# Performance work log

Hardware: AMD Instinct MI355X
Metric: run time of the kernel (lower is better)

Reference implementation:

```python
import jax, jax.numpy as jnp
import numpy as np

DIM = 512
CODEBOOK_SIZE = 8192
B, N = 4, 4096


def setup_inputs() -> dict:
    key = jax.random.key(0)
    k1, k2, k3 = jax.random.split(key, 3)
    scale = DIM ** -0.5
    x = jax.random.normal(k1, (B, N, DIM), dtype=jnp.float32)
    codebook = jax.random.normal(k2, (CODEBOOK_SIZE, DIM), dtype=jnp.float32) * scale
    W = jax.random.normal(k3, (DIM, DIM), dtype=jnp.float32) * scale  # Linear(dim, dim, bias=False) weight
    return {"x": x, "codebook": codebook, "W": W}


def reference(x, codebook, W):
    # implicit_codebook = Linear(codebook): codebook @ W.T   -> [C, D]
    implicit = codebook @ W.T

    # nearest-code search (no grad in original): squared euclidean distance
    x_sg = jax.lax.stop_gradient(x)
    imp_sg = jax.lax.stop_gradient(implicit)
    # [B, N, C] logits; ||x||^2 constant w.r.t. argmin so omitted
    d2 = jnp.sum(imp_sg * imp_sg, axis=-1) - 2.0 * jnp.einsum("bnd,cd->bnc", x_sg, imp_sg)
    indices = jnp.argmin(d2, axis=-1)  # [B, N]

    quantized = implicit[indices]  # gather [B, N, D]

    commit_loss = (
        0.25 * jnp.mean((x - jax.lax.stop_gradient(quantized)) ** 2)
        + jnp.mean((jax.lax.stop_gradient(x) - quantized) ** 2)
    )

    # straight-through estimator
    quantized_st = jax.lax.stop_gradient(quantized - x) + x
    return quantized_st, indices, commit_loss
```

## Files before the change

### kernel.cpp

```cpp
#include <hip/hip_runtime.h>
#include <stdint.h>

#define DIM 512
#define NCODE 8192
#define NTOK 16384
#define QELEMS (NTOK * DIM)
#define IDX_OFF QELEMS
#define LOSS_OFF (QELEMS + NTOK)

#define S_X 21.166666f
#define S_I 423.33334f
#define SXSI 8960.5551f
#define NQ_BIAS 131072
#define MARGIN_INT 3136

#define OFF_NORMS ((size_t)NCODE * DIM * 4)
#define OFF_XI8   (OFF_NORMS + (size_t)NCODE * 4)
#define OFF_II8   (OFF_XI8 + (size_t)NTOK * DIM)
#define OFF_CAND  (OFF_II8 + (size_t)NCODE * DIM)
#define OFF_NQ    (OFF_CAND + (size_t)NTOK * 64 * 4 * 4)

typedef short bf16x8 __attribute__((ext_vector_type(8)));
typedef float f32x4 __attribute__((ext_vector_type(4)));
typedef int   i32x4 __attribute__((ext_vector_type(4)));

__device__ inline unsigned ord32(float f) {
    unsigned u = __float_as_uint(f);
    return (u & 0x80000000u) ? ~u : (u | 0x80000000u);
}
__device__ inline unsigned short f2bf(float f) {
    unsigned u = __float_as_uint(f);
    return (unsigned short)((u + 0x7fffu + ((u >> 16) & 1u)) >> 16);
}
__device__ inline float bf2f(unsigned short h) {
    return __uint_as_float((unsigned)h << 16);
}
__device__ inline int q8(float v, float s) {
    return __float2int_rn(fminf(fmaxf(v * s, -127.f), 127.f));
}
__device__ inline void gl_lds16(const void* g, void* l) {
    __builtin_amdgcn_global_load_lds(
        (const __attribute__((address_space(1))) void*)g,
        (__attribute__((address_space(3))) void*)l, 16, 0, 0);
}

__device__ inline void leaf4(const uint4 v, unsigned r[4]) {
    const unsigned s0 = min(v.x, v.z), t0 = max(v.x, v.z);
    const unsigned s1 = min(v.y, v.w), t1 = max(v.y, v.w);
    r[0] = s0; r[1] = min(t0, s1); r[2] = max(t0, s1); r[3] = t1;
}
__device__ inline void merge44(unsigned a[4], const unsigned b[4]) {
    const unsigned h0 = min(a[0], b[3]), h1 = min(a[1], b[2]);
    const unsigned h2 = min(a[2], b[1]), h3 = min(a[3], b[0]);
    const unsigned l0 = min(h0, h2), u0 = max(h0, h2);
    const unsigned l1 = min(h1, h3), u1 = max(h1, h3);
    a[0] = min(l0, l1); a[1] = max(l0, l1);
    a[2] = min(u0, u1); a[3] = max(u0, u1);
}

__global__ void init_kernel(float* __restrict__ norms) {
    int i = blockIdx.x * blockDim.x + threadIdx.x;
    if (i < NCODE) norms[i] = 0.f;
}

__global__ void split_kernel(const float* __restrict__ src,
                             unsigned short* __restrict__ dst, int n4) {
    int i = blockIdx.x * blockDim.x + threadIdx.x;
    if (i >= n4) return;
    float4 v = ((const float4*)src)[i];
    int r = i >> 7;
    int c = (i & 127) << 2;
    unsigned short hx = f2bf(v.x), hy = f2bf(v.y), hz = f2bf(v.z), hw = f2bf(v.w);
    ushort4 hi = {hx, hy, hz, hw};
    ushort4 lo = {f2bf(v.x - bf2f(hx)), f2bf(v.y - bf2f(hy)),
                  f2bf(v.z - bf2f(hz)), f2bf(v.w - bf2f(hw))};
    *(ushort4*)(dst + (size_t)r * 1024 + c) = hi;
    *(ushort4*)(dst + (size_t)r * 1024 + 512 + c) = lo;
}

__global__ __launch_bounds__(256, 2)
void gemm_imp_kernel(const unsigned short* __restrict__ A2,
                     const unsigned short* __restrict__ B2,
                     float* __restrict__ imp, unsigned char* __restrict__ impi8,
                     float* __restrict__ norms) {
    __shared__ __align__(16) unsigned short As2[64 * 64];
    __shared__ __align__(16) unsigned short Bs2[128 * 64];
    const int tid = threadIdx.x;
    const int l = tid & 63;
    const int w = tid >> 6;
    const int row0 = blockIdx.y * 64;
    const int col0 = blockIdx.x * 128;
    const int lr = l & 15;
    const int q = l >> 4;

    const int rr8 = l >> 3;
    const int gch = (l & 7) ^ (rr8 & 7);

    const unsigned short* gA = A2 + (size_t)(row0 + w * 8 + rr8) * 1024 + gch * 8;
    const unsigned short* gB = B2 + (size_t)(col0 + w * 8 + rr8) * 1024 + gch * 8;
    unsigned short* lA = As2 + (w * 8) * 64;
    unsigned short* lB = Bs2 + (w * 8) * 64;

    f32x4 acc[4][2];
    #pragma unroll
    for (int i = 0; i < 4; ++i)
        #pragma unroll
        for (int j = 0; j < 2; ++j) acc[i][j] = (f32x4)0.f;

    for (int c = 0; c < 32; ++c) {
        const int kA = (c & 15) << 6;
        const int kB = (c < 16) ? kA : ((kA + 512) & 1023);
        #pragma unroll
        for (int s = 0; s < 2; ++s)
            gl_lds16(gA + (size_t)(s * 32) * 1024 + kA, lA + (s * 32) * 64);
        #pragma unroll
        for (int s = 0; s < 4; ++s)
            gl_lds16(gB + (size_t)(s * 32) * 1024 + kB, lB + (s * 32) * 64);
        __syncthreads();
        #pragma unroll
        for (int ks = 0; ks < 2; ++ks) {
            const int lc = ks * 4 + q;
            bf16x8 af[4], bf[2];
            #pragma unroll
            for (int i = 0; i < 4; ++i) {
                const int ra = i * 16 + lr;
                af[i] = *(const bf16x8*)(As2 + ra * 64 + ((lc ^ (ra & 7)) << 3));
            }
            #pragma unroll
            for (int j = 0; j < 2; ++j) {
                const int rb = w * 32 + j * 16 + lr;
                bf[j] = *(const bf16x8*)(Bs2 + rb * 64 + ((lc ^ (rb & 7)) << 3));
            }
            #pragma unroll
            for (int i = 0; i < 4; ++i)
                #pragma unroll
                for (int j = 0; j < 2; ++j)
                    acc[i][j] = __builtin_amdgcn_mfma_f32_16x16x32_bf16(
                        af[i], bf[j], acc[i][j], 0, 0, 0);
        }
        __syncthreads();
    }

    #pragma unroll
    for (int i = 0; i < 4; ++i) {
        float np[4] = {0.f, 0.f, 0.f, 0.f};
        #pragma unroll
        for (int j = 0; j < 2; ++j) {
            const int col = col0 + w * 32 + j * 16 + lr;
            #pragma unroll
            for (int r = 0; r < 4; ++r) {
                const int row = row0 + i * 16 + q * 4 + r;
                const float v = acc[i][j][r];
                imp[(size_t)row * DIM + col] = v;
                impi8[(size_t)row * DIM + col] = (unsigned char)(q8(v, S_I) & 0xff);
                np[r] = fmaf(v, v, np[r]);
            }
        }
        #pragma unroll
        for (int r = 0; r < 4; ++r) {
            float s = np[r];
            #pragma unroll
            for (int m = 1; m < 16; m <<= 1) s += __shfl_xor(s, m, 64);
            if (lr == 0)
                atomicAdd(&norms[row0 + i * 16 + q * 4 + r], s);
        }
    }
}

__global__ void cvtx_kernel(const float* __restrict__ src,
                            unsigned char* __restrict__ dst,
                            const float* __restrict__ norms,
                            int* __restrict__ norms_q, int n4) {
    int i = blockIdx.x * blockDim.x + threadIdx.x;
    if (i >= n4) return;
    if (i < NCODE) norms_q[i] = __float2int_rn(norms[i] * SXSI) + NQ_BIAS;
    float4 v = ((const float4*)src)[i];
    unsigned wd = (unsigned)(q8(v.x, S_X) & 0xff)
                | ((unsigned)(q8(v.y, S_X) & 0xff) << 8)
                | ((unsigned)(q8(v.z, S_X) & 0xff) << 16)
                | ((unsigned)(q8(v.w, S_X) & 0xff) << 24);
    ((unsigned*)dst)[i] = wd;
}

__global__ __launch_bounds__(256, 4)
void coarse_kernel(const unsigned char* __restrict__ Xi8,
                   const unsigned char* __restrict__ Ii8,
                   const int* __restrict__ norms_q,
                   unsigned* __restrict__ cand) {
    __shared__ __align__(16) unsigned char smem[32768];
    unsigned char* As = smem;
    unsigned char* Bsm = smem + 16384;
    unsigned* Sw = (unsigned*)smem;

    const int tid = threadIdx.x;
    const int l = tid & 63;
    const int w = tid >> 6;

    const int id = blockIdx.y * 64 + blockIdx.x;
    const int xcd = id & 7;
    const int s8 = id >> 3;
    const int bx = xcd * 8 + (s8 & 7);
    const int by = s8 >> 3;
    const int row0 = by * 128;
    const int col0 = bx * 128;

    const int wm = w & 1, wn = w >> 1;
    const int lr = l & 15;
    const int q = l >> 4;

    const int rr8 = l >> 3;
    const int ch = (l & 7) ^ (rr8 & 7);
    const unsigned char* gA = Xi8 + (size_t)(row0 + w * 32 + rr8) * DIM + ch * 16;
    const unsigned char* gB = Ii8 + (size_t)(col0 + w * 32 + rr8) * DIM + ch * 16;
    unsigned char* lA = As + (w * 32) * 128;
    unsigned char* lB = Bsm + (w * 32) * 128;

    i32x4 acc[4][4];
    #pragma unroll
    for (int i = 0; i < 4; ++i)
        #pragma unroll
        for (int j = 0; j < 4; ++j) acc[i][j] = (i32x4)0;

    for (int kc = 0; kc < DIM; kc += 128) {
        #pragma unroll
        for (int s = 0; s < 4; ++s) {
            gl_lds16(gA + (size_t)(s * 8) * DIM + kc, lA + (s * 8) * 128);
            gl_lds16(gB + (size_t)(s * 8) * DIM + kc, lB + (s * 8) * 128);
        }
        __syncthreads();
        #pragma unroll
        for (int ks = 0; ks < 2; ++ks) {
            i32x4 af[4], bfr[4];
            #pragma unroll
            for (int i = 0; i < 4; ++i)
                af[i] = *(const i32x4*)(
                    As + (wm * 64 + i * 16 + lr) * 128 +
                    (((ks * 4 + q) ^ (lr & 7)) << 4));
            #pragma unroll
            for (int j = 0; j < 4; ++j)
                bfr[j] = *(const i32x4*)(
                    Bsm + (wn * 64 + j * 16 + lr) * 128 +
                    (((ks * 4 + q) ^ (lr & 7)) << 4));
            #pragma unroll
            for (int i = 0; i < 4; ++i)
                #pragma unroll
                for (int j = 0; j < 4; ++j)
                    acc[i][j] = __builtin_amdgcn_mfma_i32_16x16x64_i8(
                        af[i], bfr[j], acc[i][j], 0, 0, 0);
        }
        __syncthreads();
    }

    int nqo[4];
    unsigned codes[4];
    #pragma unroll
    for (int j = 0; j < 4; ++j) {
        codes[j] = (unsigned)(col0 + wn * 64 + j * 16 + lr);
        nqo[j] = norms_q[codes[j]];
    }
    const int c4w = wn * 8 + (lr >> 1);
    const int wsub = (lr & 1) << 1;
    #pragma unroll
    for (int i = 0; i < 4; ++i) {
        #pragma unroll
        for (int r = 0; r < 4; ++r) {
            unsigned pv[4];
            #pragma unroll
            for (int j = 0; j < 4; ++j) {
                int d2o = nqo[j] - 2 * acc[i][j][r];
                d2o = min(max(d2o, 0), 262143);
                pv[j] = ((unsigned)d2o << 13) | codes[j];
            }
            const unsigned s1 = min(pv[0], pv[1]), g1 = max(pv[0], pv[1]);
            const unsigned s2 = min(pv[2], pv[3]), g2 = max(pv[2], pv[3]);
            uint2 o;
            o.x = min(s1, s2);
            o.y = min(max(s1, s2), min(g1, g2));
            const int tok = wm * 64 + i * 16 + q * 4 + r;
            *(uint2*)(Sw + tok * 64 + ((c4w ^ (tok & 7)) << 2) + wsub) = o;
        }
    }
    __syncthreads();

    {
        const int t = tid >> 1, h = tid & 1;
        const unsigned* rowp = Sw + t * 64;
        const int sxor = t & 7;
        unsigned a4[4], b4[4];
        {
            const uint4 va = *(const uint4*)(rowp + (((h * 8 + 0) ^ sxor) << 2));
            const uint4 vb = *(const uint4*)(rowp + (((h * 8 + 1) ^ sxor) << 2));
            leaf4(va, a4); leaf4(vb, b4); merge44(a4, b4);
        }
        #pragma unroll
        for (int p = 1; p < 4; ++p) {
            unsigned c4a[4], c4b[4];
            const uint4 va = *(const uint4*)(rowp + (((h * 8 + 2 * p) ^ sxor) << 2));
            const uint4 vb = *(const uint4*)(rowp + (((h * 8 + 2 * p + 1) ^ sxor) << 2));
            leaf4(va, c4a); leaf4(vb, c4b); merge44(c4a, c4b);
            merge44(a4, c4a);
        }
        const unsigned p0 = (unsigned)__shfl_xor((int)a4[0], 1, 64);
        const unsigned p1 = (unsigned)__shfl_xor((int)a4[1], 1, 64);
        const unsigned p2 = (unsigned)__shfl_xor((int)a4[2], 1, 64);
        const unsigned p3 = (unsigned)__shfl_xor((int)a4[3], 1, 64);
        if (!h) {
            uint4 o;
            o.x = min(a4[0], p3); o.y = min(a4[1], p2);
            o.z = min(a4[2], p1); o.w = min(a4[3], p0);
            *(uint4*)(cand + ((size_t)bx * NTOK + row0 + t) * 4) = o;
        }
    }
}

__global__ __launch_bounds__(256)
void merge_kernel(const float* __restrict__ X, const float* __restrict__ Imp,
                  const float* __restrict__ norms, const unsigned* __restrict__ cand,
                  float* __restrict__ out, float* __restrict__ lossp) {
    const int t = blockIdx.x * 4 + (threadIdx.x >> 6);
    const int l = threadIdx.x & 63;

    const uint4 c4 = *(const uint4*)(cand + ((size_t)l * NTOK + t) * 4);
    unsigned mn = min(min(c4.x, c4.y), min(c4.z, c4.w));
    #pragma unroll
    for (int o = 32; o > 0; o >>= 1)
        mn = min(mn, (unsigned)__shfl_xor((int)mn, o, 64));
    const unsigned th = (mn >> 13) + MARGIN_INT;

    const float4* xp = (const float4*)(X + (size_t)t * DIM);
    const float4 xa = xp[l * 2], xb = xp[l * 2 + 1];

    const unsigned vv[4] = {c4.x, c4.y, c4.z, c4.w};
    unsigned long long best = ~0ull;
    #pragma unroll
    for (int i = 0; i < 4; ++i) {
        const bool pass = (vv[i] >> 13) <= th;
        unsigned long long m = __ballot(pass);
        while (m) {
            const int src = __ffsll((unsigned long long)m) - 1;
            m &= m - 1;
            const int c = __shfl((int)(vv[i] & 8191u), src, 64);
            const float4* ip = (const float4*)(Imp + (size_t)c * DIM);
            const float4 ia = ip[l * 2], ib = ip[l * 2 + 1];
            float s = xa.x * ia.x + xa.y * ia.y + xa.z * ia.z + xa.w * ia.w
                    + xb.x * ib.x + xb.y * ib.y + xb.z * ib.z + xb.w * ib.w;
            #pragma unroll
            for (int o = 32; o > 0; o >>= 1) s += __shfl_xor(s, o, 64);
            const float d = fmaf(-2.f, s, norms[c]);
            const unsigned long long p =
                ((unsigned long long)ord32(d) << 32) | (unsigned)c;
            if (p < best) best = p;
        }
    }
    const int bi = (int)(best & 0xffffffffu);

    const float4* qp = (const float4*)(Imp + (size_t)bi * DIM);
    float4* op = (float4*)(out + (size_t)t * DIM);
    float ls = 0.f;
    #pragma unroll
    for (int jj = 0; jj < 2; ++jj) {
        const int j = l + jj * 64;
        const float4 qv = qp[j], xv = xp[j];
        op[j] = qv;
        const float dx = xv.x - qv.x, dy = xv.y - qv.y,
                    dz = xv.z - qv.z, dw = xv.w - qv.w;
        ls += dx * dx + dy * dy + dz * dz + dw * dw;
    }
    #pragma unroll
    for (int o = 32; o > 0; o >>= 1) ls += __shfl_xor(ls, o, 64);
    if (l == 0) {
        lossp[t] = ls;
        out[IDX_OFF + t] = (float)bi;
    }
}

__global__ __launch_bounds__(1024)
void fin_kernel(const float* __restrict__ lossp, float* __restrict__ out) {
    __shared__ float part[16];
    float s = 0.f;
    for (int i = threadIdx.x; i < NTOK; i += 1024) s += lossp[i];
    #pragma unroll
    for (int o = 32; o > 0; o >>= 1) s += __shfl_xor(s, o, 64);
    if ((threadIdx.x & 63) == 0) part[threadIdx.x >> 6] = s;
    __syncthreads();
    if (threadIdx.x == 0) {
        float tot = 0.f;
        #pragma unroll
        for (int i = 0; i < 16; ++i) tot += part[i];
        out[LOSS_OFF] = 1.25f * tot / (float)QELEMS;
    }
}

extern "C" void kernel_launch(void* const* d_in, const int* in_sizes, int n_in,
                              void* d_out, int out_size, void* d_ws, size_t ws_size,
                              hipStream_t stream) {
    const float* x  = (const float*)d_in[0];
    const float* cb = (const float*)d_in[1];
    const float* W  = (const float*)d_in[2];
    float* out = (float*)d_out;
    char* ws = (char*)d_ws;

    float* imp = (float*)ws;
    float* norms = (float*)(ws + OFF_NORMS);
    unsigned char* xi8 = (unsigned char*)(ws + OFF_XI8);
    unsigned char* ii8 = (unsigned char*)(ws + OFF_II8);
    unsigned* cand = (unsigned*)(ws + OFF_CAND);
    int* norms_q = (int*)(ws + OFF_NQ);
    unsigned short* cb2 = (unsigned short*)(ws + OFF_CAND);
    unsigned short* W2  = (unsigned short*)(ws + OFF_XI8);
    float* lossp = (float*)(ws + OFF_XI8);

    hipLaunchKernelGGL(init_kernel, dim3(NCODE / 256), dim3(256), 0, stream, norms);
    hipLaunchKernelGGL(split_kernel, dim3(NCODE * 128 / 256), dim3(256), 0, stream,
                       cb, cb2, NCODE * 128);
    hipLaunchKernelGGL(split_kernel, dim3(512 * 128 / 256), dim3(256), 0, stream,
                       W, W2, 512 * 128);
    hipLaunchKernelGGL(gemm_imp_kernel, dim3(DIM / 128, NCODE / 64), dim3(256), 0,
                       stream, cb2, W2, imp, ii8, norms);
    hipLaunchKernelGGL(cvtx_kernel, dim3(NTOK * DIM / 4 / 256), dim3(256), 0, stream,
                       x, xi8, norms, norms_q, NTOK * DIM / 4);
    hipLaunchKernelGGL(coarse_kernel, dim3(NCODE / 128, NTOK / 128), dim3(256), 0,
                       stream, xi8, ii8, norms_q, cand);
    hipLaunchKernelGGL(merge_kernel, dim3(NTOK / 4), dim3(256), 0, stream,
                       x, imp, norms, cand, out, lossp);
    hipLaunchKernelGGL(fin_kernel, dim3(1), dim3(1024), 0, stream, lossp, out);
}
```

Before: 262.2 us.

## Double-buffer int8 coarse GEMM K-loop with prefetch and new LDS layout

Restructures the int8 MFMA coarse distance kernel so the K loop runs in 64-byte chunks. The two halves of the 32KB shared buffer are ping-ponged, and the next chunk's global-to-LDS loads are issued before the current chunk's MFMAs, so load latency can hide behind compute. The load and read addressing is reworked to a paired-row swizzled layout. The launch bound hint rises from 4 to 5 blocks per CU. The epilogue now uses two lane shuffles instead of four, with both lanes writing half of the top-4 candidate result. Risks are more register pressure under the tighter occupancy bound and possible LDS bank conflicts from the new layout.

```diff
diff --git a/kernel.cpp b/kernel.cpp
--- a/kernel.cpp
+++ b/kernel.cpp
@@ -182,14 +182,12 @@
     ((unsigned*)dst)[i] = wd;
 }
 
-__global__ __launch_bounds__(256, 4)
+__global__ __launch_bounds__(256, 5)
 void coarse_kernel(const unsigned char* __restrict__ Xi8,
                    const unsigned char* __restrict__ Ii8,
                    const int* __restrict__ norms_q,
                    unsigned* __restrict__ cand) {
     __shared__ __align__(16) unsigned char smem[32768];
-    unsigned char* As = smem;
-    unsigned char* Bsm = smem + 16384;
     unsigned* Sw = (unsigned*)smem;
 
     const int tid = threadIdx.x;
@@ -208,12 +206,20 @@
     const int lr = l & 15;
     const int q = l >> 4;
 
-    const int rr8 = l >> 3;
-    const int ch = (l & 7) ^ (rr8 & 7);
-    const unsigned char* gA = Xi8 + (size_t)(row0 + w * 32 + rr8) * DIM + ch * 16;
-    const unsigned char* gB = Ii8 + (size_t)(col0 + w * 32 + rr8) * DIM + ch * 16;
-    unsigned char* lA = As + (w * 32) * 128;
-    unsigned char* lB = Bsm + (w * 32) * 128;
+    const int sl = l >> 3;
+    const int eq = (l & 7) ^ sl;
+    const int se = eq >> 2;
+    const int sq = eq & 3;
+    const unsigned char* gA0 =
+        Xi8 + (size_t)(row0 + 2 * (w * 8 + sl) + se) * DIM + sq * 16;
+    const unsigned char* gB0 =
+        Ii8 + (size_t)(col0 + 2 * (w * 8 + sl) + se) * DIM + sq * 16;
+    const int ldsA = w * 1024;
+    const int ldsB = 8192 + w * 1024;
+
+    const int p8 = ((((lr & 1) << 2) | q) ^ ((lr >> 1) & 7)) << 4;
+    const int rdA = (wm * 32 + (lr >> 1)) * 128 + p8;
+    const int rdB = 8192 + (wn * 32 + (lr >> 1)) * 128 + p8;
 
     i32x4 acc[4][4];
     #pragma unroll
@@ -221,33 +227,38 @@
         #pragma unroll
         for (int j = 0; j < 4; ++j) acc[i][j] = (i32x4)0;
 
-    for (int kc = 0; kc < DIM; kc += 128) {
-        #pragma unroll
-        for (int s = 0; s < 4; ++s) {
-            gl_lds16(gA + (size_t)(s * 8) * DIM + kc, lA + (s * 8) * 128);
-            gl_lds16(gB + (size_t)(s * 8) * DIM + kc, lB + (s * 8) * 128);
-        }
-        __syncthreads();
-        #pragma unroll
-        for (int ks = 0; ks < 2; ++ks) {
-            i32x4 af[4], bfr[4];
-            #pragma unroll
-            for (int i = 0; i < 4; ++i)
-                af[i] = *(const i32x4*)(
-                    As + (wm * 64 + i * 16 + lr) * 128 +
-                    (((ks * 4 + q) ^ (lr & 7)) << 4));
+    #pragma unroll
+    for (int s = 0; s < 2; ++s) {
+        gl_lds16(gA0 + (size_t)(s * 64) * DIM, smem + ldsA + s * 4096);
+        gl_lds16(gB0 + (size_t)(s * 64) * DIM, smem + ldsB + s * 4096);
+    }
+    __syncthreads();
+
+    #pragma unroll
+    for (int it = 0; it < 8; ++it) {
+        const int cb = (it & 1) * 16384;
+        if (it < 7) {
+            const int nb = ((it + 1) & 1) * 16384;
+            const int kc = (it + 1) << 6;
+            #pragma unroll
+            for (int s = 0; s < 2; ++s) {
+                gl_lds16(gA0 + (size_t)(s * 64) * DIM + kc, smem + nb + ldsA + s * 4096);
+                gl_lds16(gB0 + (size_t)(s * 64) * DIM + kc, smem + nb + ldsB + s * 4096);
+            }
+        }
+        i32x4 af[4], bfr[4];
+        #pragma unroll
+        for (int i = 0; i < 4; ++i)
+            af[i] = *(const i32x4*)(smem + cb + rdA + i * 1024);
+        #pragma unroll
+        for (int j = 0; j < 4; ++j)
+            bfr[j] = *(const i32x4*)(smem + cb + rdB + j * 1024);
+        #pragma unroll
+        for (int i = 0; i < 4; ++i)
             #pragma unroll
             for (int j = 0; j < 4; ++j)
-                bfr[j] = *(const i32x4*)(
-                    Bsm + (wn * 64 + j * 16 + lr) * 128 +
-                    (((ks * 4 + q) ^ (lr & 7)) << 4));
-            #pragma unroll
-            for (int i = 0; i < 4; ++i)
-                #pragma unroll
-                for (int j = 0; j < 4; ++j)
-                    acc[i][j] = __builtin_amdgcn_mfma_i32_16x16x64_i8(
-                        af[i], bfr[j], acc[i][j], 0, 0, 0);
-        }
+                acc[i][j] = __builtin_amdgcn_mfma_i32_16x16x64_i8(
+                    af[i], bfr[j], acc[i][j], 0, 0, 0);
         __syncthreads();
     }
 
@@ -300,16 +311,14 @@
             leaf4(va, c4a); leaf4(vb, c4b); merge44(c4a, c4b);
             merge44(a4, c4a);
         }
-        const unsigned p0 = (unsigned)__shfl_xor((int)a4[0], 1, 64);
-        const unsigned p1 = (unsigned)__shfl_xor((int)a4[1], 1, 64);
+        const unsigned p3 = (unsigned)__shfl_xor((int)a4[3], 1, 64);
         const unsigned p2 = (unsigned)__shfl_xor((int)a4[2], 1, 64);
-        const unsigned p3 = (unsigned)__shfl_xor((int)a4[3], 1, 64);
-        if (!h) {
-            uint4 o;
-            o.x = min(a4[0], p3); o.y = min(a4[1], p2);
-            o.z = min(a4[2], p1); o.w = min(a4[3], p0);
-            *(uint4*)(cand + ((size_t)bx * NTOK + row0 + t) * 4) = o;
-        }
+        const unsigned u0 = min(a4[0], p3);
+        const unsigned u1 = min(a4[1], p2);
+        uint2 o2;
+        o2.x = h ? u1 : u0;
+        o2.y = h ? u0 : u1;
+        *(uint2*)(cand + ((size_t)bx * NTOK + row0 + t) * 4 + h * 2) = o2;
     }
 }
 
```

Result: slower. 326.3 us (+24.4%).
